# Optimization experiments

Measured on AMD Instinct MI355X. Metric: run time of the kernel, lower is better.

The kernel has to match this reference:

```python
import jax, jax.numpy as jnp
import numpy as np

T, N, E = 2048, 11, 110
NF, EF, HID, EED, HEADS = 5, 4, 256, 32, 4
D1 = 64 * HEADS  # gat1 output dim = 256
BN_EPS = 1e-5
LN_EPS = 1e-5


def _gat(x, ea, src, dst, W, b, Wa, ba):
    """FallbackGAT: linear, gather src/dst, edge-score, softmax over ALL edges, scatter-add."""
    h = x @ W + b                                             # (N, D)
    sh, dh = h[src], h[dst]                                   # (E, D) gathers
    logits = jnp.concatenate([sh, dh, ea], axis=-1) @ Wa + ba # (E,)
    alpha = jax.nn.softmax(logits)                            # softmax over dim=0 (all edges), as in source
    return jax.ops.segment_sum(alpha[:, None] * sh, dst, num_segments=x.shape[0])


def _forward(x, edge_attr, event_embs, hx, edge_index,
             W_np, b_np, bn_g, bn_b,
             We1, be1, We2, be2,
             Wg1, bg1, Wa1, ba1,
             Wg2, bg2, Wa2, ba2,
             ln_g, ln_b,
             W_ih, W_hh, b_ih, b_hh,
             Wf, bf, Wp1, bp1, Wp2, bp2):
    src, dst = edge_index[0], edge_index[1]
    bn_inv = 1.0 / jnp.sqrt(1.0 + BN_EPS)  # eval-mode BatchNorm with running stats (0, 1)

    def step(h_state, inp):
        xt, eat, evt = inp  # (N,NF), (E,EF), (EED,)
        # node_proj: Linear -> ReLU -> BatchNorm1d (eval)
        h = jax.nn.relu(xt @ W_np + b_np)
        h = bn_g * (h * bn_inv) + bn_b
        # edge_proj: Linear -> ReLU -> Linear -> ReLU
        ea = jax.nn.relu(jax.nn.relu(eat @ We1 + be1) @ We2 + be2)
        # two GAT layers (dropout p=0)
        x1 = jax.nn.relu(_gat(h, ea, src, dst, Wg1, bg1, Wa1, ba1))
        x2 = jax.nn.relu(_gat(x1, ea, src, dst, Wg2, bg2, Wa2, ba2))
        # LayerNorm
        mu = x2.mean(-1, keepdims=True)
        var = ((x2 - mu) ** 2).mean(-1, keepdims=True)
        x2 = ln_g * (x2 - mu) / jnp.sqrt(var + LN_EPS) + ln_b
        # GRUCell (torch gate order r, z, n)
        gi = x2 @ W_ih + b_ih
        gh = h_state @ W_hh + b_hh
        ir, iz, inn = jnp.split(gi, 3, axis=-1)
        hr, hz, hn = jnp.split(gh, 3, axis=-1)
        r = jax.nn.sigmoid(ir + hr)
        z = jax.nn.sigmoid(iz + hz)
        n = jnp.tanh(inn + r * hn)
        h_new = (1.0 - z) * n + z * h_state
        # event fusion + predictor
        ev = jnp.broadcast_to(evt[None, :], (h_new.shape[0], evt.shape[0]))
        fused = jax.nn.relu(jnp.concatenate([h_new, ev], axis=-1) @ Wf + bf)
        pred = jax.nn.relu(fused @ Wp1 + bp1) @ Wp2 + bp2  # (N, 1)
        return h_new, pred

    _, preds = jax.lax.scan(step, hx, (x, edge_attr, event_embs))
    return preds  # (T, N, 1)


def setup_inputs() -> dict:
    key = jax.random.key(0)
    ks = jax.random.split(key, 20)
    def p(i, shape):
        return jax.random.normal(ks[i], shape, dtype=jnp.float32) * 0.05
    return dict(
        x=jax.random.normal(ks[0], (T, N, NF), dtype=jnp.float32),
        edge_attr=jax.random.uniform(ks[1], (T, E, EF), dtype=jnp.float32),
        event_embs=jax.random.normal(ks[2], (T, EED), dtype=jnp.float32),
        hx=jnp.zeros((N, HID), jnp.float32),
        edge_index=jax.random.randint(ks[3], (2, E), 0, N),
        W_np=p(4, (NF, 64)), b_np=jnp.zeros((64,), jnp.float32),
        bn_g=jnp.ones((64,), jnp.float32), bn_b=jnp.zeros((64,), jnp.float32),
        We1=p(5, (EF, 32)), be1=jnp.zeros((32,), jnp.float32),
        We2=p(6, (32, 16)), be2=jnp.zeros((16,), jnp.float32),
        Wg1=p(7, (64, D1)), bg1=jnp.zeros((D1,), jnp.float32),
        Wa1=p(8, (2 * D1 + 16,)), ba1=jnp.zeros((), jnp.float32),
        Wg2=p(9, (D1, HID)), bg2=jnp.zeros((HID,), jnp.float32),
        Wa2=p(10, (2 * HID + 16,)), ba2=jnp.zeros((), jnp.float32),
        ln_g=jnp.ones((HID,), jnp.float32), ln_b=jnp.zeros((HID,), jnp.float32),
        W_ih=p(11, (HID, 3 * HID)), W_hh=p(12, (HID, 3 * HID)),
        b_ih=jnp.zeros((3 * HID,), jnp.float32), b_hh=jnp.zeros((3 * HID,), jnp.float32),
        Wf=p(13, (HID + EED, HID)), bf=jnp.zeros((HID,), jnp.float32),
        Wp1=p(14, (HID, HID // 2)), bp1=jnp.zeros((HID // 2,), jnp.float32),
        Wp2=p(15, (HID // 2, 1)), bp2=jnp.zeros((1,), jnp.float32),
    )


def reference(x, edge_attr, event_embs, hx, edge_index,
              W_np, b_np, bn_g, bn_b,
              We1, be1, We2, be2,
              Wg1, bg1, Wa1, ba1,
              Wg2, bg2, Wa2, ba2,
              ln_g, ln_b,
              W_ih, W_hh, b_ih, b_hh,
              Wf, bf, Wp1, bp1, Wp2, bp2):
    return _forward(x, edge_attr, event_embs, hx, edge_index,
                    W_np, b_np, bn_g, bn_b,
                    We1, be1, We2, be2,
                    Wg1, bg1, Wa1, ba1,
                    Wg2, bg2, Wa2, ba2,
                    ln_g, ln_b,
                    W_ih, W_hh, b_ih, b_hh,
                    Wf, bf, Wp1, bp1, Wp2, bp2)
```

## Files before the change

### kernel.cpp

```cpp
#include <hip/hip_runtime.h>
#include <hip/hip_bf16.h>
#include <hip/hip_fp16.h>

#define TT   2048
#define NN   11
#define EE   110
#define NFD  5
#define EFD  4
#define HIDD 256
#define EEDD 32
#define DD1  256
#define G3   768
#define HPAD 264
#define GPT  12288
#define SLOTS 9
#define SLOTSZ (16 * HPAD)
#define FILLER_CHUNK 16384
#define FILLER_MAXCHUNKS 96

typedef __attribute__((ext_vector_type(8))) _Float16 half8v;
typedef __attribute__((ext_vector_type(8))) unsigned short ushort8v;
typedef __attribute__((ext_vector_type(4))) unsigned short ushort4v;
typedef __attribute__((ext_vector_type(4))) float float4v;

static __device__ inline unsigned short f2h(float x) {
    return __half_as_ushort(__float2half(x));
}
static __device__ inline float h2f(unsigned short v) {
    return __half2float(__ushort_as_half(v));
}
static __device__ inline float sigm_f(float x) {
    return __builtin_amdgcn_rcpf(1.f + __builtin_amdgcn_exp2f(-1.4426950408889634f * x));
}
static __device__ inline float tanh_f(float x) {
    float e = __builtin_amdgcn_exp2f(2.8853900817779268f * x);
    return 1.f - 2.f * __builtin_amdgcn_rcpf(e + 1.f);
}

__global__ __launch_bounds__(256) void precompute_kernel(
    const float* __restrict__ x, const float* __restrict__ edge_attr,
    const float* __restrict__ evs, const int* __restrict__ eidx,
    const float* __restrict__ W_np, const float* __restrict__ b_np,
    const float* __restrict__ bn_g, const float* __restrict__ bn_b,
    const float* __restrict__ We1, const float* __restrict__ be1,
    const float* __restrict__ We2, const float* __restrict__ be2,
    const float* __restrict__ Wg1, const float* __restrict__ bg1,
    const float* __restrict__ Wa1, const float* __restrict__ ba1,
    const float* __restrict__ Wg2, const float* __restrict__ bg2,
    const float* __restrict__ Wa2, const float* __restrict__ ba2,
    const float* __restrict__ ln_g, const float* __restrict__ ln_b,
    const float* __restrict__ W_ih, const float* __restrict__ b_ih,
    const float* __restrict__ Wf, const float* __restrict__ bf_,
    unsigned short* __restrict__ gi_out, float* __restrict__ evc_out)
{
    const int t   = blockIdx.x;
    const int tid = threadIdx.x;

    __shared__ __align__(16) float sh_h[NN][64];
    __shared__ __align__(16) float sh_e1[EE][32];
    __shared__ __align__(16) float sh_ea[EE][16];
    __shared__ __align__(16) float sh_h1[NN][DD1];
    __shared__ __align__(16) float sh_x[NN][DD1];
    __shared__ float sxt[NN * NFD];
    __shared__ float sev[EEDD];
    __shared__ float seat[EE * EFD];
    __shared__ float red[356];
    __shared__ float sh_s1[NN], sh_d1[NN];
    __shared__ float sh_elog[EE], sh_logit[EE], sh_alpha[EE];
    __shared__ float sh_mu[NN], sh_rs[NN];
    __shared__ float sredv[2];
    __shared__ int s_src[EE], s_dst[EE];
    __shared__ int cnt[NN], deg_start[NN + 1], e_by_dst[EE];

    if (tid < NN * NFD) sxt[tid] = x[(size_t)t * NN * NFD + tid];
    if (tid < EEDD)     sev[tid] = evs[(size_t)t * EEDD + tid];
    for (int i = tid; i < EE * EFD; i += 256)
        seat[i] = edge_attr[(size_t)t * EE * EFD + i];
    if (tid < EE) { s_src[tid] = eidx[tid]; s_dst[tid] = eidx[EE + tid]; }
    if (tid < NN) cnt[tid] = 0;
    __syncthreads();
    if (tid < EE) atomicAdd(&cnt[s_dst[tid]], 1);
    __syncthreads();
    if (tid == 0) {
        int a = 0;
        for (int n = 0; n < NN; n++) { deg_start[n] = a; a += cnt[n]; }
        deg_start[NN] = a;
    }
    __syncthreads();
    if (tid < NN) cnt[tid] = 0;
    __syncthreads();
    if (tid < EE) {
        int d = s_dst[tid];
        int pos = deg_start[d] + atomicAdd(&cnt[d], 1);
        e_by_dst[pos] = tid;
    }

    const float bn_inv = 1.0f / sqrtf(1.0f + 1e-5f);
    __syncthreads();
    for (int i = tid; i < NN * 64; i += 256) {
        int n = i >> 6, d = i & 63;
        float a = b_np[d];
        #pragma unroll
        for (int k = 0; k < NFD; k++) a += sxt[n * NFD + k] * W_np[k * 64 + d];
        a = fmaxf(a, 0.f);
        sh_h[n][d] = bn_g[d] * (a * bn_inv) + bn_b[d];
    }
    __syncthreads();

    for (int i = tid; i < EE * 32; i += 256) {
        int e = i >> 5, d = i & 31;
        float a = be1[d];
        #pragma unroll
        for (int k = 0; k < EFD; k++) a += seat[e * EFD + k] * We1[k * 32 + d];
        sh_e1[e][d] = fmaxf(a, 0.f);
    }
    __syncthreads();
    for (int i = tid; i < EE * 16; i += 256) {
        int e = i >> 4, d = i & 15;
        float a = be2[d];
        #pragma unroll
        for (int k = 0; k < 32; k++) a += sh_e1[e][k] * We2[k * 16 + d];
        sh_ea[e][d] = fmaxf(a, 0.f);
    }
    __syncthreads();

    {
        const int j = tid;
        float acc[NN];
        #pragma unroll
        for (int n = 0; n < NN; n++) acc[n] = bg1[j];
        for (int k = 0; k < 64; k += 4) {
            float w0 = Wg1[(k + 0) * DD1 + j], w1 = Wg1[(k + 1) * DD1 + j];
            float w2 = Wg1[(k + 2) * DD1 + j], w3 = Wg1[(k + 3) * DD1 + j];
            #pragma unroll
            for (int n = 0; n < NN; n++) {
                float4 hv = *(const float4*)&sh_h[n][k];
                acc[n] = fmaf(hv.w, w3, fmaf(hv.z, w2, fmaf(hv.y, w1, fmaf(hv.x, w0, acc[n]))));
            }
        }
        #pragma unroll
        for (int n = 0; n < NN; n++) sh_h1[n][j] = acc[n];
    }
    __syncthreads();
    if (tid < EE) {
        float a = ba1[0];
        #pragma unroll
        for (int k = 0; k < 16; k++) a += sh_ea[tid][k] * Wa1[2 * DD1 + k];
        sh_elog[tid] = a;
    }
    if (tid < 176) {
        int g = tid >> 3, jj = tid & 7;
        int n = (g < NN) ? g : (g - NN);
        const float* wa = (g < NN) ? Wa1 : (Wa1 + DD1);
        float s = 0.f;
        for (int k = jj; k < DD1; k += 8) s += sh_h1[n][k] * wa[k];
        red[tid] = s;
    }
    __syncthreads();
    if (tid < 22) {
        float s = 0.f;
        #pragma unroll
        for (int j2 = 0; j2 < 8; j2++) s += red[tid * 8 + j2];
        if (tid < NN) sh_s1[tid] = s; else sh_d1[tid - NN] = s;
    }
    __syncthreads();
    if (tid < EE) sh_logit[tid] = sh_s1[s_src[tid]] + sh_d1[s_dst[tid]] + sh_elog[tid];
    __syncthreads();
    if (tid < 128) red[tid] = (tid < EE) ? sh_logit[tid] : -3.0e38f;
    __syncthreads();
    for (int s = 64; s > 0; s >>= 1) {
        if (tid < s) red[tid] = fmaxf(red[tid], red[tid + s]);
        __syncthreads();
    }
    if (tid == 0) sredv[0] = red[0];
    __syncthreads();
    if (tid < 128) {
        float v = (tid < EE) ? expf(sh_logit[tid] - sredv[0]) : 0.f;
        if (tid < EE) sh_alpha[tid] = v;
        red[tid] = v;
    }
    __syncthreads();
    for (int s = 64; s > 0; s >>= 1) {
        if (tid < s) red[tid] += red[tid + s];
        __syncthreads();
    }
    if (tid == 0) sredv[1] = 1.f / red[0];
    __syncthreads();
    if (tid < EE) sh_alpha[tid] *= sredv[1];
    __syncthreads();
    for (int i = tid; i < NN * DD1; i += 256) {
        int n = i >> 8, d = i & 255;
        float a = 0.f;
        for (int p = deg_start[n]; p < deg_start[n + 1]; p++) {
            int e = e_by_dst[p];
            a += sh_alpha[e] * sh_h1[s_src[e]][d];
        }
        sh_x[n][d] = fmaxf(a, 0.f);
    }
    __syncthreads();

    {
        const int j = tid;
        float acc[NN];
        #pragma unroll
        for (int n = 0; n < NN; n++) acc[n] = bg2[j];
        for (int k = 0; k < DD1; k += 4) {
            float w0 = Wg2[(k + 0) * DD1 + j], w1 = Wg2[(k + 1) * DD1 + j];
            float w2 = Wg2[(k + 2) * DD1 + j], w3 = Wg2[(k + 3) * DD1 + j];
            #pragma unroll
            for (int n = 0; n < NN; n++) {
                float4 xv = *(const float4*)&sh_x[n][k];
                acc[n] = fmaf(xv.w, w3, fmaf(xv.z, w2, fmaf(xv.y, w1, fmaf(xv.x, w0, acc[n]))));
            }
        }
        #pragma unroll
        for (int n = 0; n < NN; n++) sh_h1[n][j] = acc[n];
    }
    __syncthreads();
    if (tid < EE) {
        float a = ba2[0];
        #pragma unroll
        for (int k = 0; k < 16; k++) a += sh_ea[tid][k] * Wa2[2 * DD1 + k];
        sh_elog[tid] = a;
    }
    if (tid < 176) {
        int g = tid >> 3, jj = tid & 7;
        int n = (g < NN) ? g : (g - NN);
        const float* wa = (g < NN) ? Wa2 : (Wa2 + DD1);
        float s = 0.f;
        for (int k = jj; k < DD1; k += 8) s += sh_h1[n][k] * wa[k];
        red[tid] = s;
    }
    __syncthreads();
    if (tid < 22) {
        float s = 0.f;
        #pragma unroll
        for (int j2 = 0; j2 < 8; j2++) s += red[tid * 8 + j2];
        if (tid < NN) sh_s1[tid] = s; else sh_d1[tid - NN] = s;
    }
    __syncthreads();
    if (tid < EE) sh_logit[tid] = sh_s1[s_src[tid]] + sh_d1[s_dst[tid]] + sh_elog[tid];
    __syncthreads();
    if (tid < 128) red[tid] = (tid < EE) ? sh_logit[tid] : -3.0e38f;
    __syncthreads();
    for (int s = 64; s > 0; s >>= 1) {
        if (tid < s) red[tid] = fmaxf(red[tid], red[tid + s]);
        __syncthreads();
    }
    if (tid == 0) sredv[0] = red[0];
    __syncthreads();
    if (tid < 128) {
        float v = (tid < EE) ? expf(sh_logit[tid] - sredv[0]) : 0.f;
        if (tid < EE) sh_alpha[tid] = v;
        red[tid] = v;
    }
    __syncthreads();
    for (int s = 64; s > 0; s >>= 1) {
        if (tid < s) red[tid] += red[tid + s];
        __syncthreads();
    }
    if (tid == 0) sredv[1] = 1.f / red[0];
    __syncthreads();
    if (tid < EE) sh_alpha[tid] *= sredv[1];
    __syncthreads();
    for (int i = tid; i < NN * DD1; i += 256) {
        int n = i >> 8, d = i & 255;
        float a = 0.f;
        for (int p = deg_start[n]; p < deg_start[n + 1]; p++) {
            int e = e_by_dst[p];
            a += sh_alpha[e] * sh_h1[s_src[e]][d];
        }
        sh_x[n][d] = fmaxf(a, 0.f);
    }
    __syncthreads();

    if (tid < 176) {
        int n = tid >> 4, jj = tid & 15;
        float s = 0.f, q = 0.f;
        for (int k = jj; k < DD1; k += 16) {
            float v = sh_x[n][k];
            s += v; q += v * v;
        }
        red[tid] = s; red[176 + tid] = q;
    }
    __syncthreads();
    if (tid < NN) {
        float s = 0.f, q = 0.f;
        #pragma unroll
        for (int j2 = 0; j2 < 16; j2++) { s += red[tid * 16 + j2]; q += red[176 + tid * 16 + j2]; }
        float mu = s * (1.f / 256.f);
        float var = q * (1.f / 256.f) - mu * mu;
        sh_mu[tid] = mu;
        sh_rs[tid] = 1.f / sqrtf(var + 1e-5f);
    }
    __syncthreads();
    for (int i = tid; i < NN * DD1; i += 256) {
        int n = i >> 8, d = i & 255;
        sh_x[n][d] = ln_g[d] * (sh_x[n][d] - sh_mu[n]) * sh_rs[n] + ln_b[d];
    }
    __syncthreads();

    {
        const int wq  = tid >> 5;
        const int fq  = (tid >> 4) & 1;
        const int lcq = tid & 15;
        #pragma unroll
        for (int c = 0; c < 3; c++) {
            const int j = tid + c * 256;
            float acc[NN];
            float bj = b_ih[j];
            #pragma unroll
            for (int n = 0; n < NN; n++) acc[n] = bj;
            for (int k = 0; k < HIDD; k += 4) {
                float w0 = W_ih[(size_t)(k + 0) * G3 + j], w1 = W_ih[(size_t)(k + 1) * G3 + j];
                float w2 = W_ih[(size_t)(k + 2) * G3 + j], w3 = W_ih[(size_t)(k + 3) * G3 + j];
                #pragma unroll
                for (int n = 0; n < NN; n++) {
                    float4 xv = *(const float4*)&sh_x[n][k];
                    acc[n] = fmaf(xv.w, w3, fmaf(xv.z, w2, fmaf(xv.y, w1, fmaf(xv.x, w0, acc[n]))));
                }
            }
            #pragma unroll
            for (int lgq = 0; lgq < 3; lgq++) {
                ushort4v v4;
                #pragma unroll
                for (int q = 0; q < 4; q++) {
                    const int n = lgq * 4 + q;
                    v4[q] = (n < NN) ? f2h(acc[n < NN ? n : 0]) : (unsigned short)0;
                }
                const int st = wq * 64 + lgq * 16 + lcq;
                *(ushort4v*)(gi_out + (size_t)t * GPT + st * 24 + c * 8 + fq * 4) = v4;
            }
        }
    }

    {
        float a = bf_[tid];
        #pragma unroll
        for (int k = 0; k < EEDD; k++) a += sev[k] * Wf[(size_t)(HIDD + k) * HIDD + tid];
        evc_out[(size_t)t * HIDD + tid] = a;
    }
}

__global__ __launch_bounds__(512, 2) void scan_mfma_kernel(
    const unsigned short* __restrict__ gip, const float* __restrict__ W_hh,
    const float* __restrict__ b_hh, const float* __restrict__ hx,
    unsigned short* __restrict__ hall16, unsigned int* flag)
{
    const int tid = threadIdx.x;

    if (blockIdx.x != 0) {
        __shared__ unsigned int lflag;
        if (tid == 0) lflag = 0;
        __syncthreads();
        float a0 = tid * 1e-8f + 0.1f, a1 = a0 + 0.01f, a2 = a0 + 0.02f, a3 = a0 + 0.03f;
        float a4 = a0 + 0.04f, a5 = a0 + 0.05f, a6 = a0 + 0.06f, a7 = a0 + 0.07f;
        for (int c = 0; c < FILLER_MAXCHUNKS; c++) {
            for (int i = 0; i < FILLER_CHUNK; i++) {
                a0 = fmaf(a0, 0.99999f, 1e-7f); a1 = fmaf(a1, 0.99999f, 1e-7f);
                a2 = fmaf(a2, 0.99999f, 1e-7f); a3 = fmaf(a3, 0.99999f, 1e-7f);
                a4 = fmaf(a4, 0.99999f, 1e-7f); a5 = fmaf(a5, 0.99999f, 1e-7f);
                a6 = fmaf(a6, 0.99999f, 1e-7f); a7 = fmaf(a7, 0.99999f, 1e-7f);
            }
            if (tid == 0) {
                if (atomicAdd(flag, 0u)) lflag = 1;
            }
            if (*(volatile unsigned int*)&lflag) break;
        }
        asm volatile("" :: "v"(a0), "v"(a1), "v"(a2), "v"(a3),
                          "v"(a4), "v"(a5), "v"(a6), "v"(a7));
        return;
    }

    const int w  = tid >> 6;
    const int l  = tid & 63;
    const int lc = l & 15;
    const int lg = l >> 4;

    __shared__ __align__(16) char smem[SLOTS * SLOTSZ * 2];
    short* sh = (short*)smem;
    float* wstage = (float*)smem;

    half8v wf[48];
    #pragma unroll
    for (int blk = 0; blk < 16; blk++) {
        __syncthreads();
        for (int i = tid; i < 16 * G3; i += 512)
            wstage[i] = W_hh[(size_t)(blk * 16) * G3 + i];
        __syncthreads();
        const int kk = blk >> 1, half = blk & 1;
        if ((lg >> 1) == half) {
            const int rbase = lg * 8 - half * 16;
            #pragma unroll
            for (int g = 0; g < 3; g++)
            #pragma unroll
            for (int f = 0; f < 2; f++) {
                const int col = g * 256 + w * 32 + f * 16 + lc;
                half8v v;
                #pragma unroll
                for (int j = 0; j < 8; j++)
                    v[j] = (_Float16)wstage[(rbase + j) * G3 + col];
                wf[kk * 6 + g * 2 + f] = v;
            }
        }
    }
    __syncthreads();

    float bias[6];
    #pragma unroll
    for (int g = 0; g < 3; g++)
    #pragma unroll
    for (int f = 0; f < 2; f++)
        bias[g * 2 + f] = b_hh[g * 256 + w * 32 + f * 16 + lc];

    for (int i = tid; i < SLOTS * SLOTSZ; i += 512) sh[i] = 0;
    __syncthreads();

    float hreg[8];
    #pragma unroll
    for (int f = 0; f < 2; f++) {
        const int u = w * 32 + f * 16 + lc;
        #pragma unroll
        for (int q = 0; q < 4; q++) {
            const int n = lg * 4 + q;
            if (n < NN) {
                float h0 = hx[n * HIDD + u];
                hreg[f * 4 + q] = h0;
                sh[0 * SLOTSZ + n * HPAD + u] = (short)f2h(h0);
            }
        }
    }
    __syncthreads();

    int rs = 0;
    for (int t = 0; t < TT; t++) {
        const int ws = (rs + 1 == SLOTS) ? 0 : rs + 1;

        const unsigned short* gp = gip + (size_t)t * GPT + tid * 24;
        ushort8v ga = *(const ushort8v*)(gp);
        ushort8v gb = *(const ushort8v*)(gp + 8);
        ushort8v gc = *(const ushort8v*)(gp + 16);

        const short* hb = sh + rs * SLOTSZ;
        float4v acc[6];
        #pragma unroll
        for (int j = 0; j < 6; j++)
            acc[j] = (float4v){bias[j], bias[j], bias[j], bias[j]};
        #pragma unroll
        for (int kk = 0; kk < 8; kk++) {
            half8v ah = *(const half8v*)&hb[lc * HPAD + kk * 32 + lg * 8];
            #pragma unroll
            for (int j = 0; j < 6; j++)
                acc[j] = __builtin_amdgcn_mfma_f32_16x16x32_f16(ah, wf[kk * 6 + j], acc[j], 0, 0, 0);
        }

        short* nh = sh + ws * SLOTSZ;
        #pragma unroll
        for (int f = 0; f < 2; f++) {
            const int u = w * 32 + f * 16 + lc;
            #pragma unroll
            for (int q = 0; q < 4; q++) {
                const int n = lg * 4 + q;
                if (n < NN) {
                    float gir = h2f(ga[f * 4 + q]);
                    float giz = h2f(gb[f * 4 + q]);
                    float gin = h2f(gc[f * 4 + q]);
                    float r   = sigm_f(gir + acc[f][q]);
                    float z   = sigm_f(giz + acc[2 + f][q]);
                    float nn_ = tanh_f(gin + r * acc[4 + f][q]);
                    float hnew = z * hreg[f * 4 + q] + (1.f - z) * nn_;
                    hreg[f * 4 + q] = hnew;
                    nh[n * HPAD + u] = (short)f2h(hnew);
                }
            }
        }

        asm volatile("s_waitcnt lgkmcnt(0)\n\ts_barrier" ::: "memory");

        if ((t & 7) == 7) {
            const int tbase = t - 7;
            int bslot = rs + 3; if (bslot >= SLOTS) bslot -= SLOTS;
            #pragma unroll
            for (int g = 0; g < 6; g++) {
                int fidx = (tid + g * 512) * 8;
                if (fidx < 8 * NN * HIDD) {
                    int tt  = fidx / (NN * HIDD);
                    int rem = fidx - tt * (NN * HIDD);
                    int n   = rem >> 8;
                    int u   = rem & 255;
                    int slot = bslot + tt; if (slot >= SLOTS) slot -= SLOTS;
                    ushort8v v = *(const ushort8v*)&((const unsigned short*)sh)[slot * SLOTSZ + n * HPAD + u];
                    *(ushort8v*)&hall16[(size_t)(tbase + tt) * (NN * HIDD) + n * HIDD + u] = v;
                }
            }
            asm volatile("s_waitcnt lgkmcnt(0)\n\ts_barrier" ::: "memory");
        }

        rs = ws;
    }

    if (tid == 0) {
        __threadfence();
        atomicExch(flag, 1u);
    }
}

__global__ __launch_bounds__(256) void predict_kernel(
    const unsigned short* __restrict__ hall16, const float* __restrict__ evc,
    const float* __restrict__ Wf, const float* __restrict__ Wp1,
    const float* __restrict__ bp1, const float* __restrict__ Wp2,
    const float* __restrict__ bp2, float* __restrict__ out)
{
    const int t = blockIdx.x, tid = threadIdx.x;
    __shared__ __align__(16) float sh[NN][HIDD];
    __shared__ __align__(16) float sf[NN][HIDD];
    __shared__ __align__(16) float sp[NN][128];
    __shared__ float red[176];

    for (int i = tid; i < NN * HIDD; i += 256)
        sh[i >> 8][i & 255] = h2f(hall16[(size_t)t * NN * HIDD + i]);
    __syncthreads();
    {
        const int j = tid;
        float acc[NN];
        float e = evc[(size_t)t * HIDD + j];
        #pragma unroll
        for (int n = 0; n < NN; n++) acc[n] = e;
        for (int k = 0; k < HIDD; k += 4) {
            float w0 = Wf[(size_t)(k + 0) * HIDD + j], w1 = Wf[(size_t)(k + 1) * HIDD + j];
            float w2 = Wf[(size_t)(k + 2) * HIDD + j], w3 = Wf[(size_t)(k + 3) * HIDD + j];
            #pragma unroll
            for (int n = 0; n < NN; n++) {
                float4 hv = *(const float4*)&sh[n][k];
                acc[n] = fmaf(hv.w, w3, fmaf(hv.z, w2, fmaf(hv.y, w1, fmaf(hv.x, w0, acc[n]))));
            }
        }
        #pragma unroll
        for (int n = 0; n < NN; n++) sf[n][j] = fmaxf(acc[n], 0.f);
    }
    __syncthreads();
    if (tid < 128) {
        float acc[NN];
        float b = bp1[tid];
        #pragma unroll
        for (int n = 0; n < NN; n++) acc[n] = b;
        for (int k = 0; k < HIDD; k += 4) {
            float w0 = Wp1[(size_t)(k + 0) * 128 + tid], w1 = Wp1[(size_t)(k + 1) * 128 + tid];
            float w2 = Wp1[(size_t)(k + 2) * 128 + tid], w3 = Wp1[(size_t)(k + 3) * 128 + tid];
            #pragma unroll
            for (int n = 0; n < NN; n++) {
                float4 fv = *(const float4*)&sf[n][k];
                acc[n] = fmaf(fv.w, w3, fmaf(fv.z, w2, fmaf(fv.y, w1, fmaf(fv.x, w0, acc[n]))));
            }
        }
        #pragma unroll
        for (int n = 0; n < NN; n++) sp[n][tid] = fmaxf(acc[n], 0.f);
    }
    __syncthreads();
    if (tid < 176) {
        int n = tid >> 4, jj = tid & 15;
        float s = 0.f;
        for (int k = jj; k < 128; k += 16) s += sp[n][k] * Wp2[k];
        red[tid] = s;
    }
    __syncthreads();
    if (tid < NN) {
        float s = 0.f;
        #pragma unroll
        for (int j2 = 0; j2 < 16; j2++) s += red[tid * 16 + j2];
        out[(size_t)t * NN + tid] = s + bp2[0];
    }
}

extern "C" void kernel_launch(void* const* d_in, const int* in_sizes, int n_in,
                              void* d_out, int out_size, void* d_ws, size_t ws_size,
                              hipStream_t stream) {
    const float* x_in  = (const float*)d_in[0];
    const float* ea_in = (const float*)d_in[1];
    const float* evs   = (const float*)d_in[2];
    const float* hx    = (const float*)d_in[3];
    const int*   eidx  = (const int*)d_in[4];
    const float* W_np  = (const float*)d_in[5];
    const float* b_np  = (const float*)d_in[6];
    const float* bn_g  = (const float*)d_in[7];
    const float* bn_b  = (const float*)d_in[8];
    const float* We1   = (const float*)d_in[9];
    const float* be1   = (const float*)d_in[10];
    const float* We2   = (const float*)d_in[11];
    const float* be2   = (const float*)d_in[12];
    const float* Wg1   = (const float*)d_in[13];
    const float* bg1   = (const float*)d_in[14];
    const float* Wa1   = (const float*)d_in[15];
    const float* ba1   = (const float*)d_in[16];
    const float* Wg2   = (const float*)d_in[17];
    const float* bg2   = (const float*)d_in[18];
    const float* Wa2   = (const float*)d_in[19];
    const float* ba2   = (const float*)d_in[20];
    const float* ln_g  = (const float*)d_in[21];
    const float* ln_b  = (const float*)d_in[22];
    const float* W_ih  = (const float*)d_in[23];
    const float* W_hh  = (const float*)d_in[24];
    const float* b_ih  = (const float*)d_in[25];
    const float* b_hh  = (const float*)d_in[26];
    const float* Wf    = (const float*)d_in[27];
    const float* bf_   = (const float*)d_in[28];
    const float* Wp1   = (const float*)d_in[29];
    const float* bp1   = (const float*)d_in[30];
    const float* Wp2   = (const float*)d_in[31];
    const float* bp2   = (const float*)d_in[32];

    unsigned short* gip = (unsigned short*)d_ws;
    float* evc = (float*)((char*)d_ws + (size_t)TT * GPT * 2);
    unsigned short* hall16 = (unsigned short*)((char*)evc + (size_t)TT * HIDD * 4);
    unsigned int* flag = (unsigned int*)((char*)hall16 + (size_t)TT * NN * HIDD * 2);

    hipMemsetAsync(flag, 0, sizeof(unsigned int), stream);

    precompute_kernel<<<TT, 256, 0, stream>>>(
        x_in, ea_in, evs, eidx,
        W_np, b_np, bn_g, bn_b, We1, be1, We2, be2,
        Wg1, bg1, Wa1, ba1, Wg2, bg2, Wa2, ba2,
        ln_g, ln_b, W_ih, b_ih, Wf, bf_, gip, evc);

    scan_mfma_kernel<<<256, 512, 0, stream>>>(gip, W_hh, b_hh, hx, hall16, flag);

    predict_kernel<<<TT, 256, 0, stream>>>(
        hall16, evc, Wf, Wp1, bp1, Wp2, bp2, (float*)d_out);
}
```

Measured before the change: 9.915 ms.

## Prefetch GRU input gates into LDS asynchronously and shrink hidden-state ring

The sequential GRU recurrence loop now streams the precomputed input-gate values for the next two timesteps into a double-buffered LDS area using global_load_lds, instead of loading them from global memory every step. This is meant to take global-load latency off the serial critical path. The hidden-state ring is reduced from 9 slots to 5 and written to global every 4 steps instead of 8, to free LDS for the gate buffers. The filler chunk count is also lowered. The vmcnt waits are hand-managed, which risks ordering errors.

```diff
diff --git a/kernel.cpp b/kernel.cpp
--- a/kernel.cpp
+++ b/kernel.cpp
@@ -13,10 +13,10 @@
 #define G3   768
 #define HPAD 264
 #define GPT  12288
-#define SLOTS 9
+#define SLOTS 5
 #define SLOTSZ (16 * HPAD)
 #define FILLER_CHUNK 16384
-#define FILLER_MAXCHUNKS 96
+#define FILLER_MAXCHUNKS 64
 
 typedef __attribute__((ext_vector_type(8))) _Float16 half8v;
 typedef __attribute__((ext_vector_type(8))) unsigned short ushort8v;
@@ -35,6 +35,10 @@
 static __device__ inline float tanh_f(float x) {
     float e = __builtin_amdgcn_exp2f(2.8853900817779268f * x);
     return 1.f - 2.f * __builtin_amdgcn_rcpf(e + 1.f);
+}
+static __device__ inline void gld16(const void* g, void* s) {
+    __builtin_amdgcn_global_load_lds((const __attribute__((address_space(1))) void*)g,
+                                     (__attribute__((address_space(3))) void*)s, 16, 0, 0);
 }
 
 __global__ __launch_bounds__(256) void precompute_kernel(
@@ -376,10 +380,11 @@
     const int l  = tid & 63;
     const int lc = l & 15;
     const int lg = l >> 4;
-
-    __shared__ __align__(16) char smem[SLOTS * SLOTSZ * 2];
-    short* sh = (short*)smem;
-    float* wstage = (float*)smem;
+    const int wu = __builtin_amdgcn_readfirstlane(w);
+
+    __shared__ short ring[SLOTS * SLOTSZ];
+    __shared__ __align__(16) unsigned short gibuf[2][2 * GPT];
+    float* wstage = (float*)&gibuf[0][0];
 
     half8v wf[48];
     #pragma unroll
@@ -406,6 +411,13 @@
     }
     __syncthreads();
 
+    #pragma unroll
+    for (int s = 0; s < 2; s++)
+    #pragma unroll
+    for (int j = 0; j < 3; j++)
+        gld16(gip + (size_t)s * GPT + (size_t)(wu * 64 + l) * 24 + j * 8,
+              &gibuf[0][s * GPT + j * 4096 + wu * 512]);
+
     float bias[6];
     #pragma unroll
     for (int g = 0; g < 3; g++)
@@ -413,7 +425,7 @@
     for (int f = 0; f < 2; f++)
         bias[g * 2 + f] = b_hh[g * 256 + w * 32 + f * 16 + lc];
 
-    for (int i = tid; i < SLOTS * SLOTSZ; i += 512) sh[i] = 0;
+    for (int i = tid; i < SLOTS * SLOTSZ; i += 512) ring[i] = 0;
     __syncthreads();
 
     float hreg[8];
@@ -426,77 +438,97 @@
             if (n < NN) {
                 float h0 = hx[n * HIDD + u];
                 hreg[f * 4 + q] = h0;
-                sh[0 * SLOTSZ + n * HPAD + u] = (short)f2h(h0);
-            }
-        }
-    }
-    __syncthreads();
+                ring[0 * SLOTSZ + n * HPAD + u] = (short)f2h(h0);
+            }
+        }
+    }
+    asm volatile("s_waitcnt lgkmcnt(0)\n\ts_barrier" ::: "memory");
 
     int rs = 0;
-    for (int t = 0; t < TT; t++) {
-        const int ws = (rs + 1 == SLOTS) ? 0 : rs + 1;
-
-        const unsigned short* gp = gip + (size_t)t * GPT + tid * 24;
-        ushort8v ga = *(const ushort8v*)(gp);
-        ushort8v gb = *(const ushort8v*)(gp + 8);
-        ushort8v gc = *(const ushort8v*)(gp + 16);
-
-        const short* hb = sh + rs * SLOTSZ;
-        float4v acc[6];
-        #pragma unroll
-        for (int j = 0; j < 6; j++)
-            acc[j] = (float4v){bias[j], bias[j], bias[j], bias[j]};
-        #pragma unroll
-        for (int kk = 0; kk < 8; kk++) {
-            half8v ah = *(const half8v*)&hb[lc * HPAD + kk * 32 + lg * 8];
+    for (int m = 0; m < TT / 2; m++) {
+        if ((m & 1) || m == 0) {
+            asm volatile("s_waitcnt vmcnt(0)" ::: "memory");
+        } else {
+            asm volatile("s_waitcnt vmcnt(3)" ::: "memory");
+        }
+
+        if (m + 1 < TT / 2) {
+            const int b = (m + 1) & 1;
+            #pragma unroll
+            for (int s = 0; s < 2; s++)
+            #pragma unroll
+            for (int j = 0; j < 3; j++)
+                gld16(gip + (size_t)(2 * (m + 1) + s) * GPT + (size_t)(wu * 64 + l) * 24 + j * 8,
+                      &gibuf[b][s * GPT + j * 4096 + wu * 512]);
+        }
+
+        #pragma unroll
+        for (int s = 0; s < 2; s++) {
+            const int t = 2 * m + s;
+            const int ws = (rs + 1 == SLOTS) ? 0 : rs + 1;
+
+            const unsigned short* gw = &gibuf[m & 1][s * GPT];
+            ushort8v ga = *(const ushort8v*)&gw[tid * 8];
+            ushort8v gb = *(const ushort8v*)&gw[4096 + tid * 8];
+            ushort8v gc = *(const ushort8v*)&gw[8192 + tid * 8];
+
+            const short* hb = ring + rs * SLOTSZ;
+            float4v acc[6];
             #pragma unroll
             for (int j = 0; j < 6; j++)
-                acc[j] = __builtin_amdgcn_mfma_f32_16x16x32_f16(ah, wf[kk * 6 + j], acc[j], 0, 0, 0);
-        }
-
-        short* nh = sh + ws * SLOTSZ;
-        #pragma unroll
-        for (int f = 0; f < 2; f++) {
-            const int u = w * 32 + f * 16 + lc;
-            #pragma unroll
-            for (int q = 0; q < 4; q++) {
-                const int n = lg * 4 + q;
-                if (n < NN) {
-                    float gir = h2f(ga[f * 4 + q]);
-                    float giz = h2f(gb[f * 4 + q]);
-                    float gin = h2f(gc[f * 4 + q]);
-                    float r   = sigm_f(gir + acc[f][q]);
-                    float z   = sigm_f(giz + acc[2 + f][q]);
-                    float nn_ = tanh_f(gin + r * acc[4 + f][q]);
-                    float hnew = z * hreg[f * 4 + q] + (1.f - z) * nn_;
-                    hreg[f * 4 + q] = hnew;
-                    nh[n * HPAD + u] = (short)f2h(hnew);
+                acc[j] = (float4v){bias[j], bias[j], bias[j], bias[j]};
+            #pragma unroll
+            for (int kk = 0; kk < 8; kk++) {
+                half8v ah = *(const half8v*)&hb[lc * HPAD + kk * 32 + lg * 8];
+                #pragma unroll
+                for (int j = 0; j < 6; j++)
+                    acc[j] = __builtin_amdgcn_mfma_f32_16x16x32_f16(ah, wf[kk * 6 + j], acc[j], 0, 0, 0);
+            }
+
+            short* nh = ring + ws * SLOTSZ;
+            #pragma unroll
+            for (int f = 0; f < 2; f++) {
+                const int u = w * 32 + f * 16 + lc;
+                #pragma unroll
+                for (int q = 0; q < 4; q++) {
+                    const int n = lg * 4 + q;
+                    if (n < NN) {
+                        float gir = h2f(ga[f * 4 + q]);
+                        float giz = h2f(gb[f * 4 + q]);
+                        float gin = h2f(gc[f * 4 + q]);
+                        float r   = sigm_f(gir + acc[f][q]);
+                        float z   = sigm_f(giz + acc[2 + f][q]);
+                        float nn_ = tanh_f(gin + r * acc[4 + f][q]);
+                        float hnew = z * hreg[f * 4 + q] + (1.f - z) * nn_;
+                        hreg[f * 4 + q] = hnew;
+                        nh[n * HPAD + u] = (short)f2h(hnew);
+                    }
                 }
             }
-        }
-
-        asm volatile("s_waitcnt lgkmcnt(0)\n\ts_barrier" ::: "memory");
-
-        if ((t & 7) == 7) {
-            const int tbase = t - 7;
-            int bslot = rs + 3; if (bslot >= SLOTS) bslot -= SLOTS;
-            #pragma unroll
-            for (int g = 0; g < 6; g++) {
-                int fidx = (tid + g * 512) * 8;
-                if (fidx < 8 * NN * HIDD) {
-                    int tt  = fidx / (NN * HIDD);
-                    int rem = fidx - tt * (NN * HIDD);
-                    int n   = rem >> 8;
-                    int u   = rem & 255;
-                    int slot = bslot + tt; if (slot >= SLOTS) slot -= SLOTS;
-                    ushort8v v = *(const ushort8v*)&((const unsigned short*)sh)[slot * SLOTSZ + n * HPAD + u];
-                    *(ushort8v*)&hall16[(size_t)(tbase + tt) * (NN * HIDD) + n * HIDD + u] = v;
+
+            asm volatile("s_waitcnt lgkmcnt(0)\n\ts_barrier" ::: "memory");
+
+            if ((t & 3) == 3) {
+                const int tbase = t - 3;
+                #pragma unroll
+                for (int g = 0; g < 3; g++) {
+                    int fidx = (tid + g * 512) * 8;
+                    if (fidx < 4 * NN * HIDD) {
+                        int tt2 = fidx / (NN * HIDD);
+                        int rem = fidx - tt2 * (NN * HIDD);
+                        int n   = rem >> 8;
+                        int u   = rem & 255;
+                        int k   = tbase + tt2;
+                        int slot = (k + 1) % SLOTS;
+                        ushort8v v = *(const ushort8v*)&((const unsigned short*)ring)[slot * SLOTSZ + n * HPAD + u];
+                        *(ushort8v*)&hall16[(size_t)k * (NN * HIDD) + n * HIDD + u] = v;
+                    }
                 }
-            }
-            asm volatile("s_waitcnt lgkmcnt(0)\n\ts_barrier" ::: "memory");
-        }
-
-        rs = ws;
+                asm volatile("s_waitcnt lgkmcnt(0)\n\ts_barrier" ::: "memory");
+            }
+
+            rs = ws;
+        }
     }
 
     if (tid == 0) {
```

New measurement: 15.95 ms. 60.8% more time.
